# Kernel tuning notes

Measured on AMD Instinct MI355X. Metric: run time of the kernel, lower is better.

Reference implementation:

```python
import jax, jax.numpy as jnp
import numpy as np

B, NINP, NCLS = 16384, 2048, 100


def setup_inputs() -> dict:
    key = jax.random.key(0)
    k1, k2, k3, k4, k5 = jax.random.split(key, 5)
    s = 1.0 / np.sqrt(NINP)
    return {
        "time_series": jax.random.normal(k1, (B, NINP), jnp.float32),
        "w_weight": jax.random.uniform(k2, (NINP, NINP), jnp.float32, -s, s),
        "w_bias": jax.random.uniform(k3, (NINP,), jnp.float32, -s, s),
        "fc_weight": jax.random.uniform(k4, (NCLS, NINP), jnp.float32, -s, s),
        "fc_bias": jax.random.uniform(k5, (NCLS,), jnp.float32, -s, s),
    }


def reference(time_series, w_weight, w_bias, fc_weight, fc_bias):
    # time_series: [B, N]
    n = time_series.shape[1]
    # gamma = cumsum(softmax(w(x), axis=1), axis=1): monotone warp in (0, 1]
    gamma = jnp.cumsum(jax.nn.softmax(time_series @ w_weight.T + w_bias, axis=1), axis=1)
    # Interp1d(linspace(0,1,N), x, gamma): per-row linear interpolation,
    # sampling each series at the warped time points gamma.
    xs = jnp.linspace(0.0, 1.0, n, dtype=time_series.dtype)  # shared knot grid
    warped = jax.vmap(lambda g, y: jnp.interp(g, xs, y))(gamma, time_series)  # [B, N]
    return warped @ fc_weight.T + fc_bias  # [B, nclasses]
```

## Files before the change

### kernel.cpp

```cpp
#include <hip/hip_runtime.h>
#include <hip/hip_bf16.h>

#define BROWS 16384
#define NDIM  2048
#define NCLS  100

typedef __attribute__((ext_vector_type(8))) __bf16 bf16x8;
typedef __attribute__((ext_vector_type(4))) float f32x4;
typedef __attribute__((ext_vector_type(16))) float f32x16;
typedef __attribute__((ext_vector_type(4))) unsigned short u16x4;
typedef __attribute__((ext_vector_type(8))) unsigned short u16x8;

__device__ __forceinline__ unsigned short f2bf(float f) {
    union { float f; unsigned int u; } v; v.f = f;
    unsigned int u = v.u;
    unsigned int r = (u + 0x7fffu + ((u >> 16) & 1u)) >> 16;
    return (unsigned short)r;
}
__device__ __forceinline__ float bf2f(unsigned short h) {
    union { unsigned int u; float f; } v; v.u = ((unsigned int)h) << 16;
    return v.f;
}

#define GLOAD_LDS(g, l) \
    __builtin_amdgcn_global_load_lds((const __attribute__((address_space(1))) void*)(g), \
                                     (__attribute__((address_space(3))) void*)(l), 16, 0, 0)

#define WAITCNT_VM(N) asm volatile("s_waitcnt vmcnt(" #N ")" ::: "memory")
#define WAITCNT_LGKM0() do { \
    asm volatile("s_waitcnt lgkmcnt(0)" ::: "memory"); \
    __builtin_amdgcn_sched_barrier(0); \
} while (0)
#define RAW_BARRIER() __builtin_amdgcn_s_barrier()

__global__ __launch_bounds__(256) void prep_kernel(const float4* __restrict__ x,
                                                   const float4* __restrict__ w,
                                                   const float4* __restrict__ f,
                                                   u16x4* __restrict__ xhi, u16x4* __restrict__ xlo,
                                                   u16x4* __restrict__ whi, u16x4* __restrict__ wlo,
                                                   u16x4* __restrict__ fdst,
                                                   int n4x, int n4w, int n4f)
{
    int i = blockIdx.x * 256 + threadIdx.x;
    if (i < n4x + n4w) {
        const float4* src; u16x4 *hi, *lo; int idx;
        if (i < n4x) { src = x; hi = xhi; lo = xlo; idx = i; }
        else { idx = i - n4x; src = w; hi = whi; lo = wlo; }
        float4 v = src[idx];
        u16x4 h, l;
        h.x = f2bf(v.x); l.x = f2bf(v.x - bf2f(h.x));
        h.y = f2bf(v.y); l.y = f2bf(v.y - bf2f(h.y));
        h.z = f2bf(v.z); l.z = f2bf(v.z - bf2f(h.z));
        h.w = f2bf(v.w); l.w = f2bf(v.w - bf2f(h.w));
        hi[idx] = h; lo[idx] = l;
    } else if (fdst != nullptr) {
        int idx = i - n4x - n4w;
        if (idx >= n4f) return;
        float4 v = f[idx];
        u16x4 h;
        h.x = f2bf(v.x); h.y = f2bf(v.y); h.z = f2bf(v.z); h.w = f2bf(v.w);
        fdst[idx] = h;
    }
}

__global__ __launch_bounds__(256) void cvt_bf16_kernel(const float4* __restrict__ src,
                                                       u16x4* __restrict__ dst, int n4)
{
    int i = blockIdx.x * 256 + threadIdx.x;
    if (i >= n4) return;
    float4 v = src[i];
    u16x4 h;
    h.x = f2bf(v.x); h.y = f2bf(v.y); h.z = f2bf(v.z); h.w = f2bf(v.w);
    dst[i] = h;
}

__global__ __launch_bounds__(512) void gemm1_mfma_fused_kernel(
        const unsigned short* __restrict__ xhi,
        const unsigned short* __restrict__ xlo,
        const unsigned short* __restrict__ whi,
        const unsigned short* __restrict__ wlo,
        const float* __restrict__ bias,
        float* __restrict__ C)
{
    __shared__ unsigned short sAh[3 * 128 * 32];
    __shared__ unsigned short sAl[3 * 128 * 32];
    __shared__ unsigned short sBh[3 * 256 * 32];
    __shared__ unsigned short sBl[3 * 256 * 32];

    const int tid  = threadIdx.x;
    const int lane = tid & 63;
    const int w    = tid >> 6;
    const int wm   = w & 1;
    const int wn   = w >> 1;
    const int m0   = blockIdx.y * 128;
    const int n0   = blockIdx.x * 256;

    const int ra = tid >> 2;
    const int qa = (tid & 3) ^ ((ra >> 1) & 3);
    const size_t a_goff = (size_t)(m0 + ra) * NDIM + qa * 8;
    const int a_lb = (w * 64) * 8;

    size_t b_goff[2]; int b_lb[2];
#pragma unroll
    for (int t = 0; t < 2; t++) {
        const int c = t * 512 + tid;
        const int r = c >> 2;
        const int q = (c & 3) ^ ((r >> 1) & 3);
        b_goff[t] = (size_t)(n0 + r) * NDIM + q * 8;
        b_lb[t]   = (t * 512 + w * 64) * 8;
    }

    const int ln32 = lane & 31;
    const int lk2  = lane >> 5;
    int offA[2][2], offB[2][2];
#pragma unroll
    for (int i = 0; i < 2; i++)
#pragma unroll
        for (int ks = 0; ks < 2; ks++) {
            const int rfa = wm * 64 + i * 32 + ln32;
            offA[i][ks] = rfa * 32 + (((2 * ks + lk2) ^ ((rfa >> 1) & 3)) * 8);
            const int rfb = wn * 64 + i * 32 + ln32;
            offB[i][ks] = rfb * 32 + (((2 * ks + lk2) ^ ((rfb >> 1) & 3)) * 8);
        }

    f32x16 acc[2][2];
#pragma unroll
    for (int i = 0; i < 2; i++)
#pragma unroll
        for (int j = 0; j < 2; j++)
#pragma unroll
            for (int r = 0; r < 16; r++) acc[i][j][r] = 0.f;

#define G1_STAGE_ALL(AOFF, BOFF, KT) do { \
    GLOAD_LDS(xhi + a_goff + (KT), &sAh[(AOFF) + a_lb]); \
    GLOAD_LDS(xlo + a_goff + (KT), &sAl[(AOFF) + a_lb]); \
    GLOAD_LDS(whi + b_goff[0] + (KT), &sBh[(BOFF) + b_lb[0]]); \
    GLOAD_LDS(whi + b_goff[1] + (KT), &sBh[(BOFF) + b_lb[1]]); \
    GLOAD_LDS(wlo + b_goff[0] + (KT), &sBl[(BOFF) + b_lb[0]]); \
    GLOAD_LDS(wlo + b_goff[1] + (KT), &sBl[(BOFF) + b_lb[1]]); \
} while (0)

    G1_STAGE_ALL(0, 0, 0);
    G1_STAGE_ALL(4096, 8192, 32);
    WAITCNT_VM(6);
    RAW_BARRIER();

    int cA = 0, cB = 0;
    int sA = 2 * 4096, sB = 2 * 8192;

    for (int kt = 0; kt < NDIM; kt += 32) {
        const int skt = (kt + 64 < NDIM) ? kt + 64 : 0;

        {
            bf16x8 ah[2], al[2], bh[2], bl[2];
#pragma unroll
            for (int i = 0; i < 2; i++) {
                ah[i] = *(const bf16x8*)&sAh[cA + offA[i][0]];
                al[i] = *(const bf16x8*)&sAl[cA + offA[i][0]];
                bh[i] = *(const bf16x8*)&sBh[cB + offB[i][0]];
                bl[i] = *(const bf16x8*)&sBl[cB + offB[i][0]];
            }
            GLOAD_LDS(xhi + a_goff + skt, &sAh[sA + a_lb]);
            GLOAD_LDS(xlo + a_goff + skt, &sAl[sA + a_lb]);
            GLOAD_LDS(whi + b_goff[0] + skt, &sBh[sB + b_lb[0]]);
            RAW_BARRIER();
            WAITCNT_LGKM0();
            __builtin_amdgcn_s_setprio(1);
#pragma unroll
            for (int i = 0; i < 2; i++)
#pragma unroll
                for (int j = 0; j < 2; j++) {
                    acc[i][j] = __builtin_amdgcn_mfma_f32_32x32x16_bf16(ah[i], bh[j], acc[i][j], 0, 0, 0);
                    acc[i][j] = __builtin_amdgcn_mfma_f32_32x32x16_bf16(ah[i], bl[j], acc[i][j], 0, 0, 0);
                    acc[i][j] = __builtin_amdgcn_mfma_f32_32x32x16_bf16(al[i], bh[j], acc[i][j], 0, 0, 0);
                }
            __builtin_amdgcn_s_setprio(0);
            RAW_BARRIER();
        }

        {
            bf16x8 ah[2], al[2], bh[2], bl[2];
#pragma unroll
            for (int i = 0; i < 2; i++) {
                ah[i] = *(const bf16x8*)&sAh[cA + offA[i][1]];
                al[i] = *(const bf16x8*)&sAl[cA + offA[i][1]];
                bh[i] = *(const bf16x8*)&sBh[cB + offB[i][1]];
                bl[i] = *(const bf16x8*)&sBl[cB + offB[i][1]];
            }
            GLOAD_LDS(whi + b_goff[1] + skt, &sBh[sB + b_lb[1]]);
            GLOAD_LDS(wlo + b_goff[0] + skt, &sBl[sB + b_lb[0]]);
            GLOAD_LDS(wlo + b_goff[1] + skt, &sBl[sB + b_lb[1]]);
            WAITCNT_VM(6);
            RAW_BARRIER();
            WAITCNT_LGKM0();
            __builtin_amdgcn_s_setprio(1);
#pragma unroll
            for (int i = 0; i < 2; i++)
#pragma unroll
                for (int j = 0; j < 2; j++) {
                    acc[i][j] = __builtin_amdgcn_mfma_f32_32x32x16_bf16(ah[i], bh[j], acc[i][j], 0, 0, 0);
                    acc[i][j] = __builtin_amdgcn_mfma_f32_32x32x16_bf16(ah[i], bl[j], acc[i][j], 0, 0, 0);
                    acc[i][j] = __builtin_amdgcn_mfma_f32_32x32x16_bf16(al[i], bh[j], acc[i][j], 0, 0, 0);
                }
            __builtin_amdgcn_s_setprio(0);
            RAW_BARRIER();
        }

        cA += 4096; if (cA == 12288) cA = 0;
        cB += 8192; if (cB == 24576) cB = 0;
        sA += 4096; if (sA == 12288) sA = 0;
        sB += 8192; if (sB == 24576) sB = 0;
    }

#undef G1_STAGE_ALL

    float bb[2];
#pragma unroll
    for (int j = 0; j < 2; j++) bb[j] = bias[n0 + wn * 64 + j * 32 + ln32];
#pragma unroll
    for (int i = 0; i < 2; i++) {
#pragma unroll
        for (int j = 0; j < 2; j++) {
            const int n = n0 + wn * 64 + j * 32 + ln32;
#pragma unroll
            for (int reg = 0; reg < 16; reg++) {
                const int m = m0 + wm * 64 + i * 32 + (reg & 3) + 8 * (reg >> 2) + 4 * lk2;
                C[(size_t)m * NDIM + n] = acc[i][j][reg] + bb[j];
            }
        }
    }
}

#define SXI(i) ((i) + ((i) >> 5))

__global__ __launch_bounds__(256) void warp_bf16_kernel(const unsigned short* __restrict__ Xhi,
                                                        const unsigned short* __restrict__ Xlo,
                                                        const float* __restrict__ L,
                                                        unsigned short* __restrict__ Wout)
{
    const int N = NDIM;
    const int row = blockIdx.x;
    const int tid = threadIdx.x;
    const int lane = tid & 63;
    const int wave = tid >> 6;

    __shared__ float s_x[NDIM + NDIM / 32];
    __shared__ float s_red[4];
    __shared__ float s_wsum[4];

    const float* lrow = L + (size_t)row * N;

    float v[8];
    {
        float4 l0 = *(const float4*)(lrow + tid * 8);
        float4 l1 = *(const float4*)(lrow + tid * 8 + 4);
        v[0] = l0.x; v[1] = l0.y; v[2] = l0.z; v[3] = l0.w;
        v[4] = l1.x; v[5] = l1.y; v[6] = l1.z; v[7] = l1.w;
        u16x8 hx = *(const u16x8*)(Xhi + (size_t)row * N + tid * 8);
        u16x8 lx = *(const u16x8*)(Xlo + (size_t)row * N + tid * 8);
        float xv[8];
#pragma unroll
        for (int j = 0; j < 8; j++) xv[j] = bf2f(hx[j]) + bf2f(lx[j]);
        const int sb = SXI(tid * 8);
        *(float4*)&s_x[sb]     = make_float4(xv[0], xv[1], xv[2], xv[3]);
        *(float4*)&s_x[sb + 4] = make_float4(xv[4], xv[5], xv[6], xv[7]);
    }

    float mx = v[0];
#pragma unroll
    for (int j = 1; j < 8; j++) mx = fmaxf(mx, v[j]);
#pragma unroll
    for (int off = 32; off > 0; off >>= 1) mx = fmaxf(mx, __shfl_down(mx, off));
    if (lane == 0) s_red[wave] = mx;
    __syncthreads();
    mx = fmaxf(fmaxf(s_red[0], s_red[1]), fmaxf(s_red[2], s_red[3]));

    float c = 0.0f;
#pragma unroll
    for (int j = 0; j < 8; j++) {
        float e = __expf(v[j] - mx);
        c += e;
        v[j] = c;
    }

    float sc = c;
#pragma unroll
    for (int off = 1; off < 64; off <<= 1) {
        float t = __shfl_up(sc, off);
        if (lane >= off) sc += t;
    }
    if (lane == 63) s_wsum[wave] = sc;
    __syncthreads();
    float base = 0.0f, total = 0.0f;
#pragma unroll
    for (int w = 0; w < 4; w++) {
        float t = s_wsum[w];
        if (w < wave) base += t;
        total += t;
    }
    const float inv = 1.0f / total;
    const float prefix = base + (sc - c);

    u16x8 o;
#pragma unroll
    for (int j = 0; j < 8; j++) {
        float g = (prefix + v[j]) * inv;
        float pos = g * (float)(N - 1);
        pos = fminf(fmaxf(pos, 0.0f), (float)(N - 1));
        int i = (int)pos;
        if (i > N - 2) i = N - 2;
        float f = pos - (float)i;
        float x0 = s_x[SXI(i)];
        float x1 = s_x[SXI(i + 1)];
        o[j] = f2bf(fmaf(f, x1 - x0, x0));
    }
    *(u16x8*)(Wout + (size_t)row * N + tid * 8) = o;
}

__global__ __launch_bounds__(256) void gemm2_mfma_kernel(
        const unsigned short* __restrict__ Wp,
        const unsigned short* __restrict__ F,
        const float* __restrict__ fb,
        float* __restrict__ out)
{
    __shared__ unsigned short sA[2 * 32 * 64];
    __shared__ unsigned short sB[2 * 128 * 64];

    const int tid  = threadIdx.x;
    const int lane = tid & 63;
    const int w    = tid >> 6;
    const int m0   = blockIdx.x * 32;

    const int ar = tid >> 3, aq = tid & 7;
    const size_t a_goff = (size_t)(m0 + ar) * NDIM + ((aq ^ (ar & 7)) * 8);
    const int a_lb = (w * 64) * 8;

    size_t b_goff[4]; int b_lb[4];
#pragma unroll
    for (int t = 0; t < 4; t++) {
        const int c = t * 256 + tid;
        const int r = c >> 3, q = c & 7;
        b_goff[t] = (size_t)(r < NCLS ? r : NCLS - 1) * NDIM + ((q ^ (r & 7)) * 8);
        b_lb[t]   = (t * 256 + w * 64) * 8;
    }

    const int lm = lane & 15;
    const int lk = lane >> 4;
    int offA[2][2], offB[2][2];
#pragma unroll
    for (int i = 0; i < 2; i++)
#pragma unroll
        for (int ks = 0; ks < 2; ks++) {
            const int r = i * 16 + lm;
            offA[i][ks] = (r * 8 + ((ks * 4 + lk) ^ (r & 7))) * 8;
            const int rb = w * 32 + i * 16 + lm;
            offB[i][ks] = (rb * 8 + ((ks * 4 + lk) ^ (rb & 7))) * 8;
        }

    f32x4 acc[2][2];
#pragma unroll
    for (int i = 0; i < 2; i++)
#pragma unroll
        for (int j = 0; j < 2; j++) acc[i][j] = (f32x4){0.f, 0.f, 0.f, 0.f};

#define G2_STAGE(B, KT) do { \
    GLOAD_LDS(Wp + a_goff + (KT), &sA[(B) * 2048 + a_lb]); \
    _Pragma("unroll") \
    for (int t = 0; t < 4; t++) GLOAD_LDS(F + b_goff[t] + (KT), &sB[(B) * 8192 + b_lb[t]]); \
} while (0)

#define G2_COMPUTE(B) do { \
    _Pragma("unroll") \
    for (int ks = 0; ks < 2; ks++) { \
        bf16x8 af[2], bfr[2]; \
        _Pragma("unroll") \
        for (int i = 0; i < 2; i++) { \
            af[i]  = *(const bf16x8*)&sA[(B) * 2048 + offA[i][ks]]; \
            bfr[i] = *(const bf16x8*)&sB[(B) * 8192 + offB[i][ks]]; \
        } \
        _Pragma("unroll") \
        for (int i = 0; i < 2; i++) \
            _Pragma("unroll") \
            for (int j = 0; j < 2; j++) \
                acc[i][j] = __builtin_amdgcn_mfma_f32_16x16x32_bf16(af[i], bfr[j], acc[i][j], 0, 0, 0); \
    } \
} while (0)

    G2_STAGE(0, 0);

    for (int kt = 0; kt < NDIM; kt += 128) {
        G2_STAGE(1, kt + 64);
        WAITCNT_VM(5);
        RAW_BARRIER();
        G2_COMPUTE(0);
        RAW_BARRIER();
        G2_STAGE(0, (kt + 128 < NDIM) ? kt + 128 : 0);
        WAITCNT_VM(5);
        RAW_BARRIER();
        G2_COMPUTE(1);
        RAW_BARRIER();
    }

#undef G2_STAGE
#undef G2_COMPUTE

    const int cn = lane & 15;
    const int rg = lane >> 4;
#pragma unroll
    for (int i = 0; i < 2; i++) {
#pragma unroll
        for (int j = 0; j < 2; j++) {
            const int n = w * 32 + j * 16 + cn;
            if (n < NCLS) {
                const float bbn = fb[n];
#pragma unroll
                for (int reg = 0; reg < 4; reg++) {
                    const int m = m0 + i * 16 + rg * 4 + reg;
                    out[(size_t)m * NCLS + n] = acc[i][j][reg] + bbn;
                }
            }
        }
    }
}

__global__ __launch_bounds__(256) void gemm1_kernel(const float* __restrict__ X,
                                                    const float* __restrict__ W,
                                                    const float* __restrict__ bias,
                                                    float* __restrict__ C)
{
    const int K = NDIM;
    __shared__ float sA[16][128];
    __shared__ float sB[16][128];
    const int tid = threadIdx.x;
    const int tx = tid & 15;
    const int ty = tid >> 4;
    const int m0 = blockIdx.y * 128;
    const int n0 = blockIdx.x * 128;
    float acc[8][8];
#pragma unroll
    for (int i = 0; i < 8; i++)
#pragma unroll
        for (int j = 0; j < 8; j++) acc[i][j] = 0.0f;
    const int s_m = tid >> 1;
    const int s_c = (tid & 1) * 8;
    const float* Ag = X + (size_t)(m0 + s_m) * K + s_c;
    const float* Bg = W + (size_t)(n0 + s_m) * K + s_c;
    for (int kt = 0; kt < K; kt += 16) {
        float4 av0 = *(const float4*)(Ag + kt);
        float4 av1 = *(const float4*)(Ag + kt + 4);
        float4 bv0 = *(const float4*)(Bg + kt);
        float4 bv1 = *(const float4*)(Bg + kt + 4);
        __syncthreads();
        sA[s_c + 0][s_m] = av0.x; sA[s_c + 1][s_m] = av0.y;
        sA[s_c + 2][s_m] = av0.z; sA[s_c + 3][s_m] = av0.w;
        sA[s_c + 4][s_m] = av1.x; sA[s_c + 5][s_m] = av1.y;
        sA[s_c + 6][s_m] = av1.z; sA[s_c + 7][s_m] = av1.w;
        sB[s_c + 0][s_m] = bv0.x; sB[s_c + 1][s_m] = bv0.y;
        sB[s_c + 2][s_m] = bv0.z; sB[s_c + 3][s_m] = bv0.w;
        sB[s_c + 4][s_m] = bv1.x; sB[s_c + 5][s_m] = bv1.y;
        sB[s_c + 6][s_m] = bv1.z; sB[s_c + 7][s_m] = bv1.w;
        __syncthreads();
#pragma unroll
        for (int k = 0; k < 16; k++) {
            float4 a0 = *(const float4*)&sA[k][ty * 8];
            float4 a1 = *(const float4*)&sA[k][ty * 8 + 4];
            float4 b0 = *(const float4*)&sB[k][tx * 8];
            float4 b1 = *(const float4*)&sB[k][tx * 8 + 4];
            float a[8] = {a0.x, a0.y, a0.z, a0.w, a1.x, a1.y, a1.z, a1.w};
            float b[8] = {b0.x, b0.y, b0.z, b0.w, b1.x, b1.y, b1.z, b1.w};
#pragma unroll
            for (int i = 0; i < 8; i++)
#pragma unroll
                for (int j = 0; j < 8; j++)
                    acc[i][j] = fmaf(a[i], b[j], acc[i][j]);
        }
    }
    float bb[8];
#pragma unroll
    for (int j = 0; j < 8; j++) bb[j] = bias[n0 + tx * 8 + j];
#pragma unroll
    for (int i = 0; i < 8; i++) {
        const int m = m0 + ty * 8 + i;
        float* crow = C + (size_t)m * NDIM + n0 + tx * 8;
        *(float4*)(crow)     = make_float4(acc[i][0] + bb[0], acc[i][1] + bb[1],
                                           acc[i][2] + bb[2], acc[i][3] + bb[3]);
        *(float4*)(crow + 4) = make_float4(acc[i][4] + bb[4], acc[i][5] + bb[5],
                                           acc[i][6] + bb[6], acc[i][7] + bb[7]);
    }
}

__global__ __launch_bounds__(256) void warp_kernel_f32(const float* __restrict__ X,
                                                       float* __restrict__ L)
{
    const int N = NDIM;
    const int row = blockIdx.x;
    const int tid = threadIdx.x;
    const int lane = tid & 63;
    const int wave = tid >> 6;
    __shared__ float s_x[NDIM];
    __shared__ float s_red[4];
    __shared__ float s_wsum[4];
    float* lrow = L + (size_t)row * N;
    const float* xrow = X + (size_t)row * N;
    float v[8];
    {
        float4 l0 = *(const float4*)(lrow + tid * 8);
        float4 l1 = *(const float4*)(lrow + tid * 8 + 4);
        v[0] = l0.x; v[1] = l0.y; v[2] = l0.z; v[3] = l0.w;
        v[4] = l1.x; v[5] = l1.y; v[6] = l1.z; v[7] = l1.w;
        float4 x0 = *(const float4*)(xrow + tid * 8);
        float4 x1 = *(const float4*)(xrow + tid * 8 + 4);
        *(float4*)&s_x[tid * 8]     = x0;
        *(float4*)&s_x[tid * 8 + 4] = x1;
    }
    float mx = v[0];
#pragma unroll
    for (int j = 1; j < 8; j++) mx = fmaxf(mx, v[j]);
#pragma unroll
    for (int off = 32; off > 0; off >>= 1) mx = fmaxf(mx, __shfl_down(mx, off));
    if (lane == 0) s_red[wave] = mx;
    __syncthreads();
    mx = fmaxf(fmaxf(s_red[0], s_red[1]), fmaxf(s_red[2], s_red[3]));
    float c = 0.0f;
#pragma unroll
    for (int j = 0; j < 8; j++) {
        float e = __expf(v[j] - mx);
        c += e;
        v[j] = c;
    }
    float sc = c;
#pragma unroll
    for (int off = 1; off < 64; off <<= 1) {
        float t = __shfl_up(sc, off);
        if (lane >= off) sc += t;
    }
    if (lane == 63) s_wsum[wave] = sc;
    __syncthreads();
    float base = 0.0f, total = 0.0f;
#pragma unroll
    for (int w = 0; w < 4; w++) {
        float t = s_wsum[w];
        if (w < wave) base += t;
        total += t;
    }
    const float inv = 1.0f / total;
    const float prefix = base + (sc - c);
    float w8[8];
#pragma unroll
    for (int j = 0; j < 8; j++) {
        float g = (prefix + v[j]) * inv;
        float pos = g * (float)(N - 1);
        pos = fminf(fmaxf(pos, 0.0f), (float)(N - 1));
        int i = (int)pos;
        if (i > N - 2) i = N - 2;
        float f = pos - (float)i;
        w8[j] = fmaf(f, s_x[i + 1] - s_x[i], s_x[i]);
    }
    *(float4*)(lrow + tid * 8)     = make_float4(w8[0], w8[1], w8[2], w8[3]);
    *(float4*)(lrow + tid * 8 + 4) = make_float4(w8[4], w8[5], w8[6], w8[7]);
}

__global__ __launch_bounds__(256) void gemm2_kernel(const float* __restrict__ Wp,
                                                    const float* __restrict__ F,
                                                    const float* __restrict__ fb,
                                                    float* __restrict__ out)
{
    const int K = NDIM;
    __shared__ float sA[16][64];
    __shared__ float sB[16][128];
    const int tid = threadIdx.x;
    const int tx = tid & 15;
    const int ty = tid >> 4;
    const int m0 = blockIdx.x * 64;
    float acc[4][8];
#pragma unroll
    for (int i = 0; i < 4; i++)
#pragma unroll
        for (int j = 0; j < 8; j++) acc[i][j] = 0.0f;
    const int a_m = tid >> 2;
    const int a_c = (tid & 3) * 4;
    const int b_n = tid >> 1;
    const int b_c = (tid & 1) * 8;
    const bool bvalid = (b_n < NCLS);
    const float* Ag = Wp + (size_t)(m0 + a_m) * K + a_c;
    const float* Bg = F + (size_t)b_n * K + b_c;
    for (int kt = 0; kt < K; kt += 16) {
        float4 av = *(const float4*)(Ag + kt);
        float4 bv0 = make_float4(0.f, 0.f, 0.f, 0.f);
        float4 bv1 = make_float4(0.f, 0.f, 0.f, 0.f);
        if (bvalid) {
            bv0 = *(const float4*)(Bg + kt);
            bv1 = *(const float4*)(Bg + kt + 4);
        }
        __syncthreads();
        sA[a_c + 0][a_m] = av.x; sA[a_c + 1][a_m] = av.y;
        sA[a_c + 2][a_m] = av.z; sA[a_c + 3][a_m] = av.w;
        sB[b_c + 0][b_n] = bv0.x; sB[b_c + 1][b_n] = bv0.y;
        sB[b_c + 2][b_n] = bv0.z; sB[b_c + 3][b_n] = bv0.w;
        sB[b_c + 4][b_n] = bv1.x; sB[b_c + 5][b_n] = bv1.y;
        sB[b_c + 6][b_n] = bv1.z; sB[b_c + 7][b_n] = bv1.w;
        __syncthreads();
#pragma unroll
        for (int k = 0; k < 16; k++) {
            float4 a4 = *(const float4*)&sA[k][ty * 4];
            float4 b0 = *(const float4*)&sB[k][tx * 8];
            float4 b1 = *(const float4*)&sB[k][tx * 8 + 4];
            float a[4] = {a4.x, a4.y, a4.z, a4.w};
            float b[8] = {b0.x, b0.y, b0.z, b0.w, b1.x, b1.y, b1.z, b1.w};
#pragma unroll
            for (int i = 0; i < 4; i++)
#pragma unroll
                for (int j = 0; j < 8; j++)
                    acc[i][j] = fmaf(a[i], b[j], acc[i][j]);
        }
    }
#pragma unroll
    for (int i = 0; i < 4; i++) {
        const int m = m0 + ty * 4 + i;
#pragma unroll
        for (int j = 0; j < 8; j++) {
            const int n = tx * 8 + j;
            if (n < NCLS) out[(size_t)m * NCLS + n] = acc[i][j] + fb[n];
        }
    }
}

extern "C" void kernel_launch(void* const* d_in, const int* in_sizes, int n_in,
                              void* d_out, int out_size, void* d_ws, size_t ws_size,
                              hipStream_t stream) {
    const float* x  = (const float*)d_in[0];
    const float* ww = (const float*)d_in[1];
    const float* wb = (const float*)d_in[2];
    const float* fw = (const float*)d_in[3];
    const float* fb = (const float*)d_in[4];
    float* out = (float*)d_out;

    char* ws = (char*)d_ws;
    float* logits = (float*)ws;
    const size_t LOGITS_B = (size_t)BROWS * NDIM * 4;
    const size_t XBF_B    = (size_t)BROWS * NDIM * 2;
    const size_t WBF_B    = (size_t)NDIM * NDIM * 2;
    const size_t FCB_B    = (size_t)NCLS * NDIM * 2;
    unsigned short* xhi = (unsigned short*)(ws + LOGITS_B);
    unsigned short* xlo = (unsigned short*)(ws + LOGITS_B + XBF_B);
    unsigned short* whi = (unsigned short*)(ws + LOGITS_B + 2 * XBF_B);
    unsigned short* wlo = (unsigned short*)(ws + LOGITS_B + 2 * XBF_B + WBF_B);
    unsigned short* fcb = (unsigned short*)(ws + LOGITS_B + 2 * XBF_B + 2 * WBF_B);
    unsigned short* wbf = xlo;
    const size_t WS_NEED  = LOGITS_B + 2 * XBF_B + 2 * WBF_B;
    const size_t WS_NEED2 = WS_NEED + FCB_B;

    const int n4x = BROWS * NDIM / 4;
    const int n4w = NDIM * NDIM / 4;
    const int n4f = NCLS * NDIM / 4;

    if (ws_size >= WS_NEED2) {
        prep_kernel<<<(n4x + n4w + n4f + 255) / 256, 256, 0, stream>>>(
            (const float4*)x, (const float4*)ww, (const float4*)fw,
            (u16x4*)xhi, (u16x4*)xlo, (u16x4*)whi, (u16x4*)wlo, (u16x4*)fcb,
            n4x, n4w, n4f);
        gemm1_mfma_fused_kernel<<<dim3(NDIM / 256, BROWS / 128), 512, 0, stream>>>(
            xhi, xlo, whi, wlo, wb, logits);
        warp_bf16_kernel<<<BROWS, 256, 0, stream>>>(xhi, xlo, logits, wbf);
        gemm2_mfma_kernel<<<BROWS / 32, 256, 0, stream>>>(wbf, fcb, fb, out);
    } else if (ws_size >= WS_NEED) {
        unsigned short* fwb = wlo;
        prep_kernel<<<(n4x + n4w + 255) / 256, 256, 0, stream>>>(
            (const float4*)x, (const float4*)ww, (const float4*)fw,
            (u16x4*)xhi, (u16x4*)xlo, (u16x4*)whi, (u16x4*)wlo, (u16x4*)nullptr,
            n4x, n4w, 0);
        gemm1_mfma_fused_kernel<<<dim3(NDIM / 256, BROWS / 128), 512, 0, stream>>>(
            xhi, xlo, whi, wlo, wb, logits);
        warp_bf16_kernel<<<BROWS, 256, 0, stream>>>(xhi, xlo, logits, wbf);
        cvt_bf16_kernel<<<(n4f + 255) / 256, 256, 0, stream>>>(
            (const float4*)fw, (u16x4*)fwb, n4f);
        gemm2_mfma_kernel<<<BROWS / 32, 256, 0, stream>>>(wbf, fwb, fb, out);
    } else {
        gemm1_kernel<<<dim3(NDIM / 128, BROWS / 128), 256, 0, stream>>>(x, ww, wb, logits);
        warp_kernel_f32<<<BROWS, 256, 0, stream>>>(x, logits);
        gemm2_kernel<<<BROWS / 64, 256, 0, stream>>>(logits, fw, fb, out);
    }
}
```

Before: 706.3 us.

## Enlarge GEMM1 block tile to 256x256 with double-buffered LDS pipeline

The first GEMM's block tile grows from 128x256 to 256x256, so each wave now computes a 128x64 output sub-tile instead of 64x64. This raises the ratio of MFMA work to LDS and global traffic per k-step. The triple-buffered, two-stage-ahead prefetch becomes a double buffer that prefetches one stage ahead and splits the A and B loads across the sub-steps. The risks are higher register pressure from twice the accumulators, half as many blocks (512) to fill the CUs, and less latency hiding from the shallower pipeline.

New measurement: 781.4 us. 1.11x slower.

```diff
diff --git a/kernel.cpp b/kernel.cpp
--- a/kernel.cpp
+++ b/kernel.cpp
@@ -82,149 +82,178 @@
         const float* __restrict__ bias,
         float* __restrict__ C)
 {
-    __shared__ unsigned short sAh[3 * 128 * 32];
-    __shared__ unsigned short sAl[3 * 128 * 32];
-    __shared__ unsigned short sBh[3 * 256 * 32];
-    __shared__ unsigned short sBl[3 * 256 * 32];
+    __shared__ unsigned short sAh[2 * 256 * 32];
+    __shared__ unsigned short sAl[2 * 256 * 32];
+    __shared__ unsigned short sBh[2 * 256 * 32];
+    __shared__ unsigned short sBl[2 * 256 * 32];
 
     const int tid  = threadIdx.x;
     const int lane = tid & 63;
     const int w    = tid >> 6;
-    const int wm   = w & 1;
-    const int wn   = w >> 1;
-    const int m0   = blockIdx.y * 128;
+    const int wm   = w >> 2;
+    const int wn   = w & 3;
+    const int m0   = blockIdx.y * 256;
     const int n0   = blockIdx.x * 256;
 
-    const int ra = tid >> 2;
-    const int qa = (tid & 3) ^ ((ra >> 1) & 3);
-    const size_t a_goff = (size_t)(m0 + ra) * NDIM + qa * 8;
-    const int a_lb = (w * 64) * 8;
-
-    size_t b_goff[2]; int b_lb[2];
+    size_t a_goff[2], b_goff[2]; int lb[2];
 #pragma unroll
     for (int t = 0; t < 2; t++) {
         const int c = t * 512 + tid;
         const int r = c >> 2;
         const int q = (c & 3) ^ ((r >> 1) & 3);
+        a_goff[t] = (size_t)(m0 + r) * NDIM + q * 8;
         b_goff[t] = (size_t)(n0 + r) * NDIM + q * 8;
-        b_lb[t]   = (t * 512 + w * 64) * 8;
+        lb[t] = (t * 512 + w * 64) * 8;
     }
 
     const int ln32 = lane & 31;
     const int lk2  = lane >> 5;
-    int offA[2][2], offB[2][2];
-#pragma unroll
-    for (int i = 0; i < 2; i++)
+    int offA[4][2], offB[2][2];
+#pragma unroll
+    for (int i = 0; i < 4; i++)
 #pragma unroll
         for (int ks = 0; ks < 2; ks++) {
-            const int rfa = wm * 64 + i * 32 + ln32;
+            const int rfa = wm * 128 + i * 32 + ln32;
             offA[i][ks] = rfa * 32 + (((2 * ks + lk2) ^ ((rfa >> 1) & 3)) * 8);
-            const int rfb = wn * 64 + i * 32 + ln32;
-            offB[i][ks] = rfb * 32 + (((2 * ks + lk2) ^ ((rfb >> 1) & 3)) * 8);
-        }
-
-    f32x16 acc[2][2];
-#pragma unroll
-    for (int i = 0; i < 2; i++)
+        }
+#pragma unroll
+    for (int j = 0; j < 2; j++)
+#pragma unroll
+        for (int ks = 0; ks < 2; ks++) {
+            const int rfb = wn * 64 + j * 32 + ln32;
+            offB[j][ks] = rfb * 32 + (((2 * ks + lk2) ^ ((rfb >> 1) & 3)) * 8);
+        }
+
+    f32x16 acc[4][2];
+#pragma unroll
+    for (int i = 0; i < 4; i++)
 #pragma unroll
         for (int j = 0; j < 2; j++)
 #pragma unroll
             for (int r = 0; r < 16; r++) acc[i][j][r] = 0.f;
 
-#define G1_STAGE_ALL(AOFF, BOFF, KT) do { \
-    GLOAD_LDS(xhi + a_goff + (KT), &sAh[(AOFF) + a_lb]); \
-    GLOAD_LDS(xlo + a_goff + (KT), &sAl[(AOFF) + a_lb]); \
-    GLOAD_LDS(whi + b_goff[0] + (KT), &sBh[(BOFF) + b_lb[0]]); \
-    GLOAD_LDS(whi + b_goff[1] + (KT), &sBh[(BOFF) + b_lb[1]]); \
-    GLOAD_LDS(wlo + b_goff[0] + (KT), &sBl[(BOFF) + b_lb[0]]); \
-    GLOAD_LDS(wlo + b_goff[1] + (KT), &sBl[(BOFF) + b_lb[1]]); \
+#define G1_STAGE_A(SB, KT) do { \
+    GLOAD_LDS(xhi + a_goff[0] + (KT), &sAh[(SB) + lb[0]]); \
+    GLOAD_LDS(xhi + a_goff[1] + (KT), &sAh[(SB) + lb[1]]); \
+    GLOAD_LDS(xlo + a_goff[0] + (KT), &sAl[(SB) + lb[0]]); \
+    GLOAD_LDS(xlo + a_goff[1] + (KT), &sAl[(SB) + lb[1]]); \
 } while (0)
-
-    G1_STAGE_ALL(0, 0, 0);
-    G1_STAGE_ALL(4096, 8192, 32);
-    WAITCNT_VM(6);
+#define G1_STAGE_B(SB, KT) do { \
+    GLOAD_LDS(whi + b_goff[0] + (KT), &sBh[(SB) + lb[0]]); \
+    GLOAD_LDS(whi + b_goff[1] + (KT), &sBh[(SB) + lb[1]]); \
+    GLOAD_LDS(wlo + b_goff[0] + (KT), &sBl[(SB) + lb[0]]); \
+    GLOAD_LDS(wlo + b_goff[1] + (KT), &sBl[(SB) + lb[1]]); \
+} while (0)
+
+#define MFMA3(ACC, AH, AL, BH, BL) do { \
+    ACC = __builtin_amdgcn_mfma_f32_32x32x16_bf16(AH, BH, ACC, 0, 0, 0); \
+    ACC = __builtin_amdgcn_mfma_f32_32x32x16_bf16(AH, BL, ACC, 0, 0, 0); \
+    ACC = __builtin_amdgcn_mfma_f32_32x32x16_bf16(AL, BH, ACC, 0, 0, 0); \
+} while (0)
+
+    G1_STAGE_A(0, 0);
+    G1_STAGE_B(0, 0);
+    WAITCNT_VM(0);
     RAW_BARRIER();
 
-    int cA = 0, cB = 0;
-    int sA = 2 * 4096, sB = 2 * 8192;
-
+    int cb = 0;
     for (int kt = 0; kt < NDIM; kt += 32) {
-        const int skt = (kt + 64 < NDIM) ? kt + 64 : 0;
+        const int skt = (kt + 32 < NDIM) ? kt + 32 : 0;
+        const int sb = cb ^ 8192;
 
         {
-            bf16x8 ah[2], al[2], bh[2], bl[2];
-#pragma unroll
-            for (int i = 0; i < 2; i++) {
-                ah[i] = *(const bf16x8*)&sAh[cA + offA[i][0]];
-                al[i] = *(const bf16x8*)&sAl[cA + offA[i][0]];
-                bh[i] = *(const bf16x8*)&sBh[cB + offB[i][0]];
-                bl[i] = *(const bf16x8*)&sBl[cB + offB[i][0]];
+            bf16x8 bh0 = *(const bf16x8*)&sBh[cb + offB[0][0]];
+            bf16x8 bh1 = *(const bf16x8*)&sBh[cb + offB[1][0]];
+            bf16x8 bl0 = *(const bf16x8*)&sBl[cb + offB[0][0]];
+            bf16x8 bl1 = *(const bf16x8*)&sBl[cb + offB[1][0]];
+            {
+                bf16x8 ah0 = *(const bf16x8*)&sAh[cb + offA[0][0]];
+                bf16x8 ah1 = *(const bf16x8*)&sAh[cb + offA[1][0]];
+                bf16x8 al0 = *(const bf16x8*)&sAl[cb + offA[0][0]];
+                bf16x8 al1 = *(const bf16x8*)&sAl[cb + offA[1][0]];
+                G1_STAGE_A(sb, skt);
+                RAW_BARRIER();
+                WAITCNT_LGKM0();
+                __builtin_amdgcn_s_setprio(1);
+                MFMA3(acc[0][0], ah0, al0, bh0, bl0);
+                MFMA3(acc[0][1], ah0, al0, bh1, bl1);
+                MFMA3(acc[1][0], ah1, al1, bh0, bl0);
+                MFMA3(acc[1][1], ah1, al1, bh1, bl1);
+                __builtin_amdgcn_s_setprio(0);
+                RAW_BARRIER();
             }
-            GLOAD_LDS(xhi + a_goff + skt, &sAh[sA + a_lb]);
-            GLOAD_LDS(xlo + a_goff + skt, &sAl[sA + a_lb]);
-            GLOAD_LDS(whi + b_goff[0] + skt, &sBh[sB + b_lb[0]]);
-            RAW_BARRIER();
-            WAITCNT_LGKM0();
-            __builtin_amdgcn_s_setprio(1);
-#pragma unroll
-            for (int i = 0; i < 2; i++)
-#pragma unroll
-                for (int j = 0; j < 2; j++) {
-                    acc[i][j] = __builtin_amdgcn_mfma_f32_32x32x16_bf16(ah[i], bh[j], acc[i][j], 0, 0, 0);
-                    acc[i][j] = __builtin_amdgcn_mfma_f32_32x32x16_bf16(ah[i], bl[j], acc[i][j], 0, 0, 0);
-                    acc[i][j] = __builtin_amdgcn_mfma_f32_32x32x16_bf16(al[i], bh[j], acc[i][j], 0, 0, 0);
-                }
-            __builtin_amdgcn_s_setprio(0);
-            RAW_BARRIER();
-        }
-
+            {
+                bf16x8 ah2 = *(const bf16x8*)&sAh[cb + offA[2][0]];
+                bf16x8 ah3 = *(const bf16x8*)&sAh[cb + offA[3][0]];
+                bf16x8 al2 = *(const bf16x8*)&sAl[cb + offA[2][0]];
+                bf16x8 al3 = *(const bf16x8*)&sAl[cb + offA[3][0]];
+                G1_STAGE_B(sb, skt);
+                RAW_BARRIER();
+                WAITCNT_LGKM0();
+                __builtin_amdgcn_s_setprio(1);
+                MFMA3(acc[2][0], ah2, al2, bh0, bl0);
+                MFMA3(acc[2][1], ah2, al2, bh1, bl1);
+                MFMA3(acc[3][0], ah3, al3, bh0, bl0);
+                MFMA3(acc[3][1], ah3, al3, bh1, bl1);
+                __builtin_amdgcn_s_setprio(0);
+                RAW_BARRIER();
+            }
+        }
         {
-            bf16x8 ah[2], al[2], bh[2], bl[2];
-#pragma unroll
-            for (int i = 0; i < 2; i++) {
-                ah[i] = *(const bf16x8*)&sAh[cA + offA[i][1]];
-                al[i] = *(const bf16x8*)&sAl[cA + offA[i][1]];
-                bh[i] = *(const bf16x8*)&sBh[cB + offB[i][1]];
-                bl[i] = *(const bf16x8*)&sBl[cB + offB[i][1]];
+            bf16x8 bh0 = *(const bf16x8*)&sBh[cb + offB[0][1]];
+            bf16x8 bh1 = *(const bf16x8*)&sBh[cb + offB[1][1]];
+            bf16x8 bl0 = *(const bf16x8*)&sBl[cb + offB[0][1]];
+            bf16x8 bl1 = *(const bf16x8*)&sBl[cb + offB[1][1]];
+            {
+                bf16x8 ah0 = *(const bf16x8*)&sAh[cb + offA[0][1]];
+                bf16x8 ah1 = *(const bf16x8*)&sAh[cb + offA[1][1]];
+                bf16x8 al0 = *(const bf16x8*)&sAl[cb + offA[0][1]];
+                bf16x8 al1 = *(const bf16x8*)&sAl[cb + offA[1][1]];
+                RAW_BARRIER();
+                WAITCNT_LGKM0();
+                __builtin_amdgcn_s_setprio(1);
+                MFMA3(acc[0][0], ah0, al0, bh0, bl0);
+                MFMA3(acc[0][1], ah0, al0, bh1, bl1);
+                MFMA3(acc[1][0], ah1, al1, bh0, bl0);
+                MFMA3(acc[1][1], ah1, al1, bh1, bl1);
+                __builtin_amdgcn_s_setprio(0);
+                RAW_BARRIER();
             }
-            GLOAD_LDS(whi + b_goff[1] + skt, &sBh[sB + b_lb[1]]);
-            GLOAD_LDS(wlo + b_goff[0] + skt, &sBl[sB + b_lb[0]]);
-            GLOAD_LDS(wlo + b_goff[1] + skt, &sBl[sB + b_lb[1]]);
-            WAITCNT_VM(6);
-            RAW_BARRIER();
-            WAITCNT_LGKM0();
-            __builtin_amdgcn_s_setprio(1);
-#pragma unroll
-            for (int i = 0; i < 2; i++)
-#pragma unroll
-                for (int j = 0; j < 2; j++) {
-                    acc[i][j] = __builtin_amdgcn_mfma_f32_32x32x16_bf16(ah[i], bh[j], acc[i][j], 0, 0, 0);
-                    acc[i][j] = __builtin_amdgcn_mfma_f32_32x32x16_bf16(ah[i], bl[j], acc[i][j], 0, 0, 0);
-                    acc[i][j] = __builtin_amdgcn_mfma_f32_32x32x16_bf16(al[i], bh[j], acc[i][j], 0, 0, 0);
-                }
-            __builtin_amdgcn_s_setprio(0);
-            RAW_BARRIER();
-        }
-
-        cA += 4096; if (cA == 12288) cA = 0;
-        cB += 8192; if (cB == 24576) cB = 0;
-        sA += 4096; if (sA == 12288) sA = 0;
-        sB += 8192; if (sB == 24576) sB = 0;
-    }
-
-#undef G1_STAGE_ALL
+            {
+                bf16x8 ah2 = *(const bf16x8*)&sAh[cb + offA[2][1]];
+                bf16x8 ah3 = *(const bf16x8*)&sAh[cb + offA[3][1]];
+                bf16x8 al2 = *(const bf16x8*)&sAl[cb + offA[2][1]];
+                bf16x8 al3 = *(const bf16x8*)&sAl[cb + offA[3][1]];
+                WAITCNT_VM(0);
+                RAW_BARRIER();
+                WAITCNT_LGKM0();
+                __builtin_amdgcn_s_setprio(1);
+                MFMA3(acc[2][0], ah2, al2, bh0, bl0);
+                MFMA3(acc[2][1], ah2, al2, bh1, bl1);
+                MFMA3(acc[3][0], ah3, al3, bh0, bl0);
+                MFMA3(acc[3][1], ah3, al3, bh1, bl1);
+                __builtin_amdgcn_s_setprio(0);
+                RAW_BARRIER();
+            }
+        }
+        cb = sb;
+    }
+
+#undef G1_STAGE_A
+#undef G1_STAGE_B
+#undef MFMA3
 
     float bb[2];
 #pragma unroll
     for (int j = 0; j < 2; j++) bb[j] = bias[n0 + wn * 64 + j * 32 + ln32];
 #pragma unroll
-    for (int i = 0; i < 2; i++) {
+    for (int i = 0; i < 4; i++) {
 #pragma unroll
         for (int j = 0; j < 2; j++) {
             const int n = n0 + wn * 64 + j * 32 + ln32;
 #pragma unroll
             for (int reg = 0; reg < 16; reg++) {
-                const int m = m0 + wm * 64 + i * 32 + (reg & 3) + 8 * (reg >> 2) + 4 * lk2;
+                const int m = m0 + wm * 128 + i * 32 + (reg & 3) + 8 * (reg >> 2) + 4 * lk2;
                 C[(size_t)m * NDIM + n] = acc[i][j][reg] + bb[j];
             }
         }
@@ -659,7 +688,7 @@
             (const float4*)x, (const float4*)ww, (const float4*)fw,
             (u16x4*)xhi, (u16x4*)xlo, (u16x4*)whi, (u16x4*)wlo, (u16x4*)fcb,
             n4x, n4w, n4f);
-        gemm1_mfma_fused_kernel<<<dim3(NDIM / 256, BROWS / 128), 512, 0, stream>>>(
+        gemm1_mfma_fused_kernel<<<dim3(NDIM / 256, BROWS / 256), 512, 0, stream>>>(
             xhi, xlo, whi, wlo, wb, logits);
         warp_bf16_kernel<<<BROWS, 256, 0, stream>>>(xhi, xlo, logits, wbf);
         gemm2_mfma_kernel<<<BROWS / 32, 256, 0, stream>>>(wbf, fcb, fb, out);
@@ -669,7 +698,7 @@
             (const float4*)x, (const float4*)ww, (const float4*)fw,
             (u16x4*)xhi, (u16x4*)xlo, (u16x4*)whi, (u16x4*)wlo, (u16x4*)nullptr,
             n4x, n4w, 0);
-        gemm1_mfma_fused_kernel<<<dim3(NDIM / 256, BROWS / 128), 512, 0, stream>>>(
+        gemm1_mfma_fused_kernel<<<dim3(NDIM / 256, BROWS / 256), 512, 0, stream>>>(
             xhi, xlo, whi, wlo, wb, logits);
         warp_bf16_kernel<<<BROWS, 256, 0, stream>>>(xhi, xlo, logits, wbf);
         cvt_bf16_kernel<<<(n4f + 255) / 256, 256, 0, stream>>>(
```
